# Kernel optimization log

Measured on AMD Instinct MI355X. Metric: run time of the kernel, lower is better.

## Reference

```python
import jax, jax.numpy as jnp
import numpy as np
import math

HEAD_SIZE = 64
N_EMBED = 1024
BLOCK_SIZE = 2048
BATCH = 8


def setup_inputs() -> dict:
    key = jax.random.key(0)
    k1, k2, k3, k4, k5 = jax.random.split(key, 5)
    index = jax.random.normal(k1, (BATCH, BLOCK_SIZE, N_EMBED), dtype=jnp.float32)
    memory = jax.random.normal(k2, (BATCH, BLOCK_SIZE, N_EMBED), dtype=jnp.float32)
    # torch Linear weights: [out_features, in_features], kaiming-uniform-ish init
    bound = 1.0 / math.sqrt(N_EMBED)
    Wq = jax.random.uniform(k3, (HEAD_SIZE, N_EMBED), jnp.float32, -bound, bound)
    Wk = jax.random.uniform(k4, (HEAD_SIZE, N_EMBED), jnp.float32, -bound, bound)
    Wv = jax.random.uniform(k5, (HEAD_SIZE, N_EMBED), jnp.float32, -bound, bound)
    return {"index": index, "memory": memory, "Wq": Wq, "Wk": Wk, "Wv": Wv}


def reference(index, memory, Wq, Wk, Wv):
    # q/k/v projections (Linear without bias: x @ W.T)
    q = jnp.einsum('btc,hc->bth', index, Wq)   # [B,T,H]
    k = jnp.einsum('bsc,hc->bsh', memory, Wk)  # [B,S,H]
    v = jnp.einsum('bsc,hc->bsh', memory, Wv)  # [B,S,H]
    scale = 1.0 / math.sqrt(HEAD_SIZE)
    w = jnp.einsum('bth,bsh->bts', q, k) * scale  # [B,T,S]
    # causal mask: tril==0 -> -inf
    T = index.shape[1]
    causal = jnp.tril(jnp.ones((BLOCK_SIZE, BLOCK_SIZE), dtype=bool))[:T, :T]
    w = jnp.where(causal, w, -jnp.inf)
    w = jax.nn.softmax(w, axis=-1)
    out = jnp.einsum('bts,bsh->bth', w, v)  # [B,T,H]
    return out
```

## Files before the change

kernel.cpp:

```cpp
#include <hip/hip_runtime.h>
#include <math.h>

typedef __bf16 bf16;
typedef __bf16 bf16x4 __attribute__((ext_vector_type(4)));
typedef __bf16 bf16x8 __attribute__((ext_vector_type(8)));
typedef float f32x4 __attribute__((ext_vector_type(4)));

#define MFMA16(a,b,c) __builtin_amdgcn_mfma_f32_16x16x32_bf16((a),(b),(c),0,0,0)

static constexpr int HS  = 64;
static constexpr int SEQ = 2048;
static constexpr int NE  = 1024;
static constexpr int NB  = 8;

__device__ __forceinline__ bf16x8 cvt8(float4 a, float4 b) {
  bf16x8 r;
  r[0]=(bf16)a.x; r[1]=(bf16)a.y; r[2]=(bf16)a.z; r[3]=(bf16)a.w;
  r[4]=(bf16)b.x; r[5]=(bf16)b.y; r[6]=(bf16)b.z; r[7]=(bf16)b.w;
  return r;
}

__device__ __forceinline__ void gload16(const void* g, void* l) {
  __builtin_amdgcn_global_load_lds(
      (const __attribute__((address_space(1))) void*)g,
      (__attribute__((address_space(3))) void*)l, 16, 0, 0);
}

__global__ __launch_bounds__(256) void wcvt_kernel(
    const float* __restrict__ Wq, const float* __restrict__ Wk,
    const float* __restrict__ Wv, bf16* __restrict__ wqb,
    bf16* __restrict__ wkb, bf16* __restrict__ wvb)
{
  int i = (blockIdx.x * 256 + threadIdx.x) * 4;
  float4 q = *(const float4*)(Wq + i);
  float4 k = *(const float4*)(Wk + i);
  float4 v = *(const float4*)(Wv + i);
  bf16x4 qo, ko, vo;
  qo[0]=(bf16)(q.x*0.125f); qo[1]=(bf16)(q.y*0.125f); qo[2]=(bf16)(q.z*0.125f); qo[3]=(bf16)(q.w*0.125f);
  ko[0]=(bf16)k.x; ko[1]=(bf16)k.y; ko[2]=(bf16)k.z; ko[3]=(bf16)k.w;
  vo[0]=(bf16)v.x; vo[1]=(bf16)v.y; vo[2]=(bf16)v.z; vo[3]=(bf16)v.w;
  *(bf16x4*)(wqb + i) = qo;
  *(bf16x4*)(wkb + i) = ko;
  *(bf16x4*)(wvb + i) = vo;
}

template<int KV>
__device__ __forceinline__ void proj_body(
    const float* __restrict__ X, const bf16* __restrict__ W0,
    const bf16* __restrict__ W1, bf16* __restrict__ out0,
    bf16* __restrict__ outVT, int slab,
    char* Xs0, char* Xs1, char* W0s0, char* W0s1, char* W1s0, char* W1s1)
{
  const int tid  = threadIdx.x;
  const int lane = tid & 63;
  const int w    = tid >> 6;
  const int m    = lane & 15;
  const int g    = lane >> 4;
  const int rowBase = slab * 64;

  const f32x4 vz = {0.f,0.f,0.f,0.f};
  f32x4 accA[4] = {vz, vz, vz, vz};
  f32x4 accB[4] = {vz, vz, vz, vz};

  const float* Xbase = X + (size_t)rowBase * NE;

  auto stage = [&](int kt, char* Xd, char* W0d, char* W1d) {
#pragma unroll
    for (int q = 0; q < 4; ++q) {
      int r = (q*4 + w)*4 + (lane >> 4);
      int s = lane & 15;
      const float* src = Xbase + (size_t)r * NE + kt*64 + ((s ^ (r & 15)) * 4);
      gload16(src, Xd + (q*4 + w)*1024);
    }
#pragma unroll
    for (int q = 0; q < 2; ++q) {
      int r = (q*4 + w)*8 + (lane >> 3);
      int s = lane & 7;
      size_t soff = (size_t)r * NE + kt*64 + ((s ^ (r & 7)) * 8);
      gload16(W0 + soff, W0d + (q*4 + w)*1024);
      if (KV) gload16(W1 + soff, W1d + (q*4 + w)*1024);
    }
  };

  auto compute = [&](const char* Xd, const char* W0d, const char* W1d) {
#pragma unroll
    for (int kk = 0; kk < 2; ++kk) {
      const int arow = 16*w + m;
      const int s0 = 2*(kk*4 + g);
      const char* ab = Xd + arow*256;
      float4 x0 = *(const float4*)(ab + (( s0      ^ (arow & 15)) * 16));
      float4 x1 = *(const float4*)(ab + (((s0 + 1) ^ (arow & 15)) * 16));
      bf16x8 af = cvt8(x0, x1);
#pragma unroll
      for (int n = 0; n < 4; ++n) {
        const int col = 16*n + m;
        const int ws  = kk*4 + g;
        bf16x8 b0 = *(const bf16x8*)(W0d + col*128 + ((ws ^ (col & 7)) * 16));
        accA[n] = MFMA16(af, b0, accA[n]);
        if (KV) {
          bf16x8 b1 = *(const bf16x8*)(W1d + col*128 + ((ws ^ (col & 7)) * 16));
          accB[n] = MFMA16(af, b1, accB[n]);
        }
      }
    }
  };

  stage(0, Xs0, W0s0, W1s0);
  stage(1, Xs1, W0s1, W1s1);
#pragma unroll
  for (int t = 0; t < 16; ++t) {
    if (t < 15) {
      if (KV) asm volatile("s_waitcnt vmcnt(8)" ::: "memory");
      else    asm volatile("s_waitcnt vmcnt(6)" ::: "memory");
    } else {
      asm volatile("s_waitcnt vmcnt(0)" ::: "memory");
    }
    __builtin_amdgcn_s_barrier();
    __builtin_amdgcn_sched_barrier(0);
    if ((t & 1) == 0) compute(Xs0, W0s0, W1s0);
    else              compute(Xs1, W0s1, W1s1);
    __builtin_amdgcn_sched_barrier(0);
    __builtin_amdgcn_s_barrier();
    if (t + 2 < 16) {
      if ((t & 1) == 0) stage(t + 2, Xs0, W0s0, W1s0);
      else              stage(t + 2, Xs1, W0s1, W1s1);
    }
  }

#pragma unroll
  for (int n = 0; n < 4; ++n)
#pragma unroll
    for (int i = 0; i < 4; ++i) {
      int row = rowBase + 16*w + 4*g + i;
      int h   = 16*n + m;
      out0[(size_t)row * HS + h] = (bf16)accA[n][i];
      if (KV)
        outVT[((size_t)(row >> 11) * HS + h) * SEQ + (row & 2047)] =
            (bf16)accB[n][i];
    }
}

__global__ __launch_bounds__(256, 2) void proj_kernel(
    const float* __restrict__ index, const float* __restrict__ memory,
    const bf16* __restrict__ wqb, const bf16* __restrict__ wkb,
    const bf16* __restrict__ wvb, bf16* __restrict__ qb,
    bf16* __restrict__ kb, bf16* __restrict__ vtb)
{
  __shared__ __align__(1024) char Xs0[16384], Xs1[16384];
  __shared__ __align__(1024) char W0s0[8192], W0s1[8192];
  __shared__ __align__(1024) char W1s0[8192], W1s1[8192];
  if (blockIdx.x < 256)
    proj_body<0>(index,  wqb, nullptr, qb, nullptr, blockIdx.x,
                 Xs0, Xs1, W0s0, W0s1, W1s0, W1s1);
  else
    proj_body<1>(memory, wkb, wvb,     kb, vtb, blockIdx.x - 256,
                 Xs0, Xs1, W0s0, W0s1, W1s0, W1s1);
}

__global__ __launch_bounds__(128) void attn_kernel(
    const bf16* __restrict__ qb, const bf16* __restrict__ kb,
    const bf16* __restrict__ vtb, float* __restrict__ out)
{
  __shared__ __align__(16) bf16 Ks[2][64][72];
  __shared__ __align__(16) bf16 VTs[2][64][72];
  __shared__ __align__(16) bf16 Ps[2][16][72];

  const int tid  = threadIdx.x;
  const int lane = tid & 63;
  const int w    = tid >> 6;
  const int m    = lane & 15;
  const int g    = lane >> 4;
  const int qt   = 127 - blockIdx.x;
  const int b    = blockIdx.y;
  const int nkv  = (qt >> 2) + 1;
  const int r0   = lane >> 1;
  const int hh   = (lane & 1) * 32;

  bf16x8 qf0 = *(const bf16x8*)(qb + ((size_t)b*SEQ + qt*16 + m)*HS + g*8);
  bf16x8 qf1 = *(const bf16x8*)(qb + ((size_t)b*SEQ + qt*16 + m)*HS + 32 + g*8);

  const f32x4 vz = {0.f,0.f,0.f,0.f};
  f32x4 o_acc[4] = {vz, vz, vz, vz};
  float mrun = -INFINITY, lrun = 0.f;

  bf16x8 kp[8], vp[8];
  const bf16* kbB = kb  + (size_t)b*SEQ*HS;
  const bf16* vtB = vtb + (size_t)b*HS*SEQ;

  auto loadKV = [&](int j) {
    const bf16* kt_ = kbB + (size_t)j*64*HS;
    const bf16* vt_ = vtB + j*64;
#pragma unroll
    for (int q = 0; q < 4; ++q) {
      kp[q]   = *(const bf16x8*)(kt_ + (size_t)r0*64        + hh + q*8);
      kp[4+q] = *(const bf16x8*)(kt_ + (size_t)(r0+32)*64   + hh + q*8);
      vp[q]   = *(const bf16x8*)(vt_ + (size_t)r0*SEQ       + hh + q*8);
      vp[4+q] = *(const bf16x8*)(vt_ + (size_t)(r0+32)*SEQ  + hh + q*8);
    }
  };
  auto writeKV = [&]() {
#pragma unroll
    for (int q = 0; q < 4; ++q) {
      *(bf16x8*)&Ks[w][r0][hh + q*8]      = kp[q];
      *(bf16x8*)&Ks[w][r0+32][hh + q*8]   = kp[4+q];
      *(bf16x8*)&VTs[w][r0][hh + q*8]     = vp[q];
      *(bf16x8*)&VTs[w][r0+32][hh + q*8]  = vp[4+q];
    }
  };

  int j = w;
  if (j < nkv) {
    loadKV(j);
    writeKV();
    while (true) {
      const int jn = j + 2;
      const bool more = jn < nkv;
      if (more) loadKV(jn);

      f32x4 s_acc[4];
#pragma unroll
      for (int na = 0; na < 4; ++na) {
        f32x4 z = vz;
        z = MFMA16(*(const bf16x8*)&Ks[w][16*na + m][g*8],      qf0, z);
        z = MFMA16(*(const bf16x8*)&Ks[w][16*na + m][32 + g*8], qf1, z);
        s_acc[na] = z;
      }
      if (j == nkv - 1) {
        const int q_ = qt*16 + m;
#pragma unroll
        for (int na = 0; na < 4; ++na)
#pragma unroll
          for (int i = 0; i < 4; ++i)
            if (j*64 + 16*na + 4*g + i > q_) s_acc[na][i] = -INFINITY;
      }

      float mx = fmaxf(
        fmaxf(fmaxf(fmaxf(s_acc[0][0],s_acc[0][1]),fmaxf(s_acc[0][2],s_acc[0][3])),
              fmaxf(fmaxf(s_acc[1][0],s_acc[1][1]),fmaxf(s_acc[1][2],s_acc[1][3]))),
        fmaxf(fmaxf(fmaxf(s_acc[2][0],s_acc[2][1]),fmaxf(s_acc[2][2],s_acc[2][3])),
              fmaxf(fmaxf(s_acc[3][0],s_acc[3][1]),fmaxf(s_acc[3][2],s_acc[3][3]))));
      mx = fmaxf(mx, __shfl_xor(mx, 16));
      mx = fmaxf(mx, __shfl_xor(mx, 32));
      float mnew = fmaxf(mrun, mx);
      float corr = __expf(mrun - mnew);
      mrun = mnew;
      float ts = 0.f;
#pragma unroll
      for (int na = 0; na < 4; ++na) {
        bf16x4 pk;
#pragma unroll
        for (int i = 0; i < 4; ++i) {
          float p = __expf(s_acc[na][i] - mnew);
          ts += p;
          pk[i] = (bf16)p;
        }
        *(bf16x4*)&Ps[w][m][16*na + 4*g] = pk;
      }
      ts += __shfl_xor(ts, 16);
      ts += __shfl_xor(ts, 32);
      lrun = lrun * corr + ts;
#pragma unroll
      for (int nd = 0; nd < 4; ++nd)
#pragma unroll
        for (int i = 0; i < 4; ++i) o_acc[nd][i] *= corr;

      bf16x8 pf0 = *(const bf16x8*)&Ps[w][m][g*8];
      bf16x8 pf1 = *(const bf16x8*)&Ps[w][m][32 + g*8];
#pragma unroll
      for (int nd = 0; nd < 4; ++nd) {
        o_acc[nd] = MFMA16(*(const bf16x8*)&VTs[w][16*nd + m][g*8],      pf0, o_acc[nd]);
        o_acc[nd] = MFMA16(*(const bf16x8*)&VTs[w][16*nd + m][32 + g*8], pf1, o_acc[nd]);
      }

      if (!more) break;
      writeKV();
      j = jn;
    }
  }

  float* PO = (float*)&Ks[w][0][0];
  float* PM = (float*)&VTs[w][0][0];
#pragma unroll
  for (int nd = 0; nd < 4; ++nd)
    *(f32x4*)&PO[m*68 + 16*nd + 4*g] = o_acc[nd];
  if (g == 0) { PM[m] = mrun; PM[16 + m] = lrun; }
  __syncthreads();

  {
    const int r  = tid >> 3;
    const int c0 = (tid & 7) * 8;
    const float* O0 = (const float*)&Ks[0][0][0];
    const float* O1 = (const float*)&Ks[1][0][0];
    const float* M0 = (const float*)&VTs[0][0][0];
    const float* M1 = (const float*)&VTs[1][0][0];
    float m0 = M0[r], l0 = M0[16 + r];
    float m1 = M1[r], l1 = M1[16 + r];
    float mx = fmaxf(m0, m1);
    float s0 = __expf(m0 - mx), s1 = __expf(m1 - mx);
    float inv = 1.f / (s0*l0 + s1*l1);
    float4 x0 = *(const float4*)(O0 + r*68 + c0);
    float4 x1 = *(const float4*)(O0 + r*68 + c0 + 4);
    float4 y0 = *(const float4*)(O1 + r*68 + c0);
    float4 y1 = *(const float4*)(O1 + r*68 + c0 + 4);
    float4 o0, o1;
    o0.x=(x0.x*s0+y0.x*s1)*inv; o0.y=(x0.y*s0+y0.y*s1)*inv;
    o0.z=(x0.z*s0+y0.z*s1)*inv; o0.w=(x0.w*s0+y0.w*s1)*inv;
    o1.x=(x1.x*s0+y1.x*s1)*inv; o1.y=(x1.y*s0+y1.y*s1)*inv;
    o1.z=(x1.z*s0+y1.z*s1)*inv; o1.w=(x1.w*s0+y1.w*s1)*inv;
    float* op = out + ((size_t)b*SEQ + qt*16 + r) * HS + c0;
    *(float4*)(op)     = o0;
    *(float4*)(op + 4) = o1;
  }
}

extern "C" void kernel_launch(void* const* d_in, const int* in_sizes, int n_in,
                              void* d_out, int out_size, void* d_ws, size_t ws_size,
                              hipStream_t stream) {
  (void)in_sizes; (void)n_in; (void)out_size; (void)ws_size;
  const float* index  = (const float*)d_in[0];
  const float* memory = (const float*)d_in[1];
  const float* Wq     = (const float*)d_in[2];
  const float* Wk     = (const float*)d_in[3];
  const float* Wv     = (const float*)d_in[4];
  float* out = (float*)d_out;

  bf16* qb  = (bf16*)d_ws;
  bf16* kb  = qb  + (size_t)NB * SEQ * HS;
  bf16* vtb = kb  + (size_t)NB * SEQ * HS;
  bf16* wqb = vtb + (size_t)NB * SEQ * HS;
  bf16* wkb = wqb + (size_t)HS * NE;
  bf16* wvb = wkb + (size_t)HS * NE;

  wcvt_kernel<<<dim3(64), 256, 0, stream>>>(Wq, Wk, Wv, wqb, wkb, wvb);
  proj_kernel<<<dim3(512), 256, 0, stream>>>(index, memory, wqb, wkb, wvb, qb, kb, vtb);
  attn_kernel<<<dim3(128, 8), 128, 0, stream>>>(qb, kb, vtb, out);
}
```

Before: 72.86 us.

## Stage projection tiles through registers with bf16 conversion and triple-buffered LDS

The projection kernel no longer uses direct global-to-LDS loads of fp32 X tiles. It now loads X and weights into registers, converts X to bf16 before writing it to LDS, and uses a three-stage LDS ring with register double-buffering. This halves the LDS footprint of X, removes the per-compute fp32-to-bf16 conversion, and drops one barrier per iteration. In exchange it uses more VGPRs and the stores go through registers, which may reduce overlap or occupancy.

```diff
diff --git a/kernel.cpp b/kernel.cpp
--- a/kernel.cpp
+++ b/kernel.cpp
@@ -18,12 +18,6 @@
   r[0]=(bf16)a.x; r[1]=(bf16)a.y; r[2]=(bf16)a.z; r[3]=(bf16)a.w;
   r[4]=(bf16)b.x; r[5]=(bf16)b.y; r[6]=(bf16)b.z; r[7]=(bf16)b.w;
   return r;
-}
-
-__device__ __forceinline__ void gload16(const void* g, void* l) {
-  __builtin_amdgcn_global_load_lds(
-      (const __attribute__((address_space(1))) void*)g,
-      (__attribute__((address_space(3))) void*)l, 16, 0, 0);
 }
 
 __global__ __launch_bounds__(256) void wcvt_kernel(
@@ -49,7 +43,9 @@
     const float* __restrict__ X, const bf16* __restrict__ W0,
     const bf16* __restrict__ W1, bf16* __restrict__ out0,
     bf16* __restrict__ outVT, int slab,
-    char* Xs0, char* Xs1, char* W0s0, char* W0s1, char* W1s0, char* W1s1)
+    char* Xs0, char* Xs1, char* Xs2,
+    char* W0s0, char* W0s1, char* W0s2,
+    char* W1s0, char* W1s1, char* W1s2)
 {
   const int tid  = threadIdx.x;
   const int lane = tid & 63;
@@ -57,75 +53,88 @@
   const int m    = lane & 15;
   const int g    = lane >> 4;
   const int rowBase = slab * 64;
+  const int srow = tid >> 2;
+  const int sg2  = (tid & 3) * 2;
+
+  const float* Xrow  = X  + (size_t)(rowBase + srow) * NE + (tid & 3) * 16;
+  const bf16*  W0row = W0 + (size_t)srow * NE + (tid & 3) * 16;
+  const bf16*  W1row = KV ? (W1 + (size_t)srow * NE + (tid & 3) * 16) : nullptr;
 
   const f32x4 vz = {0.f,0.f,0.f,0.f};
   f32x4 accA[4] = {vz, vz, vz, vz};
   f32x4 accB[4] = {vz, vz, vz, vz};
 
-  const float* Xbase = X + (size_t)rowBase * NE;
-
-  auto stage = [&](int kt, char* Xd, char* W0d, char* W1d) {
-#pragma unroll
-    for (int q = 0; q < 4; ++q) {
-      int r = (q*4 + w)*4 + (lane >> 4);
-      int s = lane & 15;
-      const float* src = Xbase + (size_t)r * NE + kt*64 + ((s ^ (r & 15)) * 4);
-      gload16(src, Xd + (q*4 + w)*1024);
-    }
-#pragma unroll
-    for (int q = 0; q < 2; ++q) {
-      int r = (q*4 + w)*8 + (lane >> 3);
-      int s = lane & 7;
-      size_t soff = (size_t)r * NE + kt*64 + ((s ^ (r & 7)) * 8);
-      gload16(W0 + soff, W0d + (q*4 + w)*1024);
-      if (KV) gload16(W1 + soff, W1d + (q*4 + w)*1024);
-    }
-  };
+  float4 xaA, xbA, xcA, xdA;  bf16x8 w0aA, w0bA, w1aA, w1bA;
+  float4 xaB, xbB, xcB, xdB;  bf16x8 w0aB, w0bB, w1aB, w1bB;
+
+#define LOAD_SET(S, kt) do {                                          \
+    const float* _xp = Xrow + (kt) * 64;                              \
+    xa##S = *(const float4*)(_xp);      xb##S = *(const float4*)(_xp + 4);  \
+    xc##S = *(const float4*)(_xp + 8);  xd##S = *(const float4*)(_xp + 12); \
+    const bf16* _w0 = W0row + (kt) * 64;                              \
+    w0a##S = *(const bf16x8*)(_w0);     w0b##S = *(const bf16x8*)(_w0 + 8); \
+    if (KV) { const bf16* _w1 = W1row + (kt) * 64;                    \
+      w1a##S = *(const bf16x8*)(_w1);   w1b##S = *(const bf16x8*)(_w1 + 8); } \
+  } while (0)
+
+#define WRITE_SET(S, Xd, W0d, W1d) do {                               \
+    *(bf16x8*)((Xd)  + srow*128 + 16*(( sg2   ) ^ (srow & 7))) = cvt8(xa##S, xb##S); \
+    *(bf16x8*)((Xd)  + srow*128 + 16*(( sg2+1 ) ^ (srow & 7))) = cvt8(xc##S, xd##S); \
+    *(bf16x8*)((W0d) + srow*128 + 16*(( sg2   ) ^ (srow & 7))) = w0a##S; \
+    *(bf16x8*)((W0d) + srow*128 + 16*(( sg2+1 ) ^ (srow & 7))) = w0b##S; \
+    if (KV) {                                                          \
+      *(bf16x8*)((W1d) + srow*128 + 16*(( sg2   ) ^ (srow & 7))) = w1a##S; \
+      *(bf16x8*)((W1d) + srow*128 + 16*(( sg2+1 ) ^ (srow & 7))) = w1b##S; \
+    }                                                                  \
+  } while (0)
 
   auto compute = [&](const char* Xd, const char* W0d, const char* W1d) {
 #pragma unroll
     for (int kk = 0; kk < 2; ++kk) {
       const int arow = 16*w + m;
-      const int s0 = 2*(kk*4 + g);
-      const char* ab = Xd + arow*256;
-      float4 x0 = *(const float4*)(ab + (( s0      ^ (arow & 15)) * 16));
-      float4 x1 = *(const float4*)(ab + (((s0 + 1) ^ (arow & 15)) * 16));
-      bf16x8 af = cvt8(x0, x1);
+      const int s = kk*4 + g;
+      bf16x8 af = *(const bf16x8*)(Xd + arow*128 + 16*(s ^ (arow & 7)));
 #pragma unroll
       for (int n = 0; n < 4; ++n) {
         const int col = 16*n + m;
-        const int ws  = kk*4 + g;
-        bf16x8 b0 = *(const bf16x8*)(W0d + col*128 + ((ws ^ (col & 7)) * 16));
+        bf16x8 b0 = *(const bf16x8*)(W0d + col*128 + 16*(s ^ (col & 7)));
         accA[n] = MFMA16(af, b0, accA[n]);
         if (KV) {
-          bf16x8 b1 = *(const bf16x8*)(W1d + col*128 + ((ws ^ (col & 7)) * 16));
+          bf16x8 b1 = *(const bf16x8*)(W1d + col*128 + 16*(s ^ (col & 7)));
           accB[n] = MFMA16(af, b1, accB[n]);
         }
       }
     }
   };
 
-  stage(0, Xs0, W0s0, W1s0);
-  stage(1, Xs1, W0s1, W1s1);
+  char* const XB[3]  = {Xs0,  Xs1,  Xs2};
+  char* const W0B[3] = {W0s0, W0s1, W0s2};
+  char* const W1B[3] = {W1s0, W1s1, W1s2};
+
+  LOAD_SET(A, 0);
+  LOAD_SET(B, 1);
+  WRITE_SET(A, XB[0], W0B[0], W1B[0]);
+  LOAD_SET(A, 2);
+
 #pragma unroll
   for (int t = 0; t < 16; ++t) {
+    const int wb = (t + 1) % 3;
     if (t < 15) {
-      if (KV) asm volatile("s_waitcnt vmcnt(8)" ::: "memory");
-      else    asm volatile("s_waitcnt vmcnt(6)" ::: "memory");
-    } else {
-      asm volatile("s_waitcnt vmcnt(0)" ::: "memory");
-    }
+      if (((t + 1) & 1) == 0) WRITE_SET(A, XB[wb], W0B[wb], W1B[wb]);
+      else                    WRITE_SET(B, XB[wb], W0B[wb], W1B[wb]);
+    }
+    if (t + 3 < 16) {
+      if (((t + 3) & 1) == 0) LOAD_SET(A, t + 3);
+      else                    LOAD_SET(B, t + 3);
+    }
+    __builtin_amdgcn_sched_barrier(0);
+    asm volatile("s_waitcnt lgkmcnt(0)" ::: "memory");
     __builtin_amdgcn_s_barrier();
     __builtin_amdgcn_sched_barrier(0);
-    if ((t & 1) == 0) compute(Xs0, W0s0, W1s0);
-    else              compute(Xs1, W0s1, W1s1);
-    __builtin_amdgcn_sched_barrier(0);
-    __builtin_amdgcn_s_barrier();
-    if (t + 2 < 16) {
-      if ((t & 1) == 0) stage(t + 2, Xs0, W0s0, W1s0);
-      else              stage(t + 2, Xs1, W0s1, W1s1);
-    }
+    compute(XB[t % 3], W0B[t % 3], W1B[t % 3]);
   }
+#undef LOAD_SET
+#undef WRITE_SET
 
 #pragma unroll
   for (int n = 0; n < 4; ++n)
@@ -146,15 +155,15 @@
     const bf16* __restrict__ wvb, bf16* __restrict__ qb,
     bf16* __restrict__ kb, bf16* __restrict__ vtb)
 {
-  __shared__ __align__(1024) char Xs0[16384], Xs1[16384];
-  __shared__ __align__(1024) char W0s0[8192], W0s1[8192];
-  __shared__ __align__(1024) char W1s0[8192], W1s1[8192];
+  __shared__ __align__(16) char Xs0[8192],  Xs1[8192],  Xs2[8192];
+  __shared__ __align__(16) char W0s0[8192], W0s1[8192], W0s2[8192];
+  __shared__ __align__(16) char W1s0[8192], W1s1[8192], W1s2[8192];
   if (blockIdx.x < 256)
     proj_body<0>(index,  wqb, nullptr, qb, nullptr, blockIdx.x,
-                 Xs0, Xs1, W0s0, W0s1, W1s0, W1s1);
+                 Xs0, Xs1, Xs2, W0s0, W0s1, W0s2, W1s0, W1s1, W1s2);
   else
     proj_body<1>(memory, wkb, wvb,     kb, vtb, blockIdx.x - 256,
-                 Xs0, Xs1, W0s0, W0s1, W1s0, W1s1);
+                 Xs0, Xs1, Xs2, W0s0, W0s1, W0s2, W1s0, W1s1, W1s2);
 }
 
 __global__ __launch_bounds__(128) void attn_kernel(
```

New measurement: 74.25 us. No clear change (+1.9%).

## Restructure projection kernel with register-staged bf16 LDS tiles and 128-row blocks

Applied to the files above, without the earlier changes.

The Q/K/V projection kernel drops direct global-to-LDS fp32 loads. Each thread now loads fp32 X tiles into registers, converts them to bf16, and writes them into swizzled LDS, with two register buffers and two LDS buffers double-buffered. Blocks grow to 512 threads covering 128 rows. In KV blocks, waves 0-3 compute K and waves 4-7 compute V, and Q and KV blocks are interleaved across the grid. The aim is to halve LDS footprint and traffic, move conversion out of the MFMA inner loop, and improve load balance. The cost is higher register pressure, fewer and larger blocks, and global-load latency hidden only by register prefetch.

```diff
diff --git a/kernel.cpp b/kernel.cpp
--- a/kernel.cpp
+++ b/kernel.cpp
@@ -13,17 +13,11 @@
 static constexpr int NE  = 1024;
 static constexpr int NB  = 8;
 
-__device__ __forceinline__ bf16x8 cvt8(float4 a, float4 b) {
+__device__ __forceinline__ bf16x8 cvt8v(f32x4 a, f32x4 b) {
   bf16x8 r;
-  r[0]=(bf16)a.x; r[1]=(bf16)a.y; r[2]=(bf16)a.z; r[3]=(bf16)a.w;
-  r[4]=(bf16)b.x; r[5]=(bf16)b.y; r[6]=(bf16)b.z; r[7]=(bf16)b.w;
+  r[0]=(bf16)a[0]; r[1]=(bf16)a[1]; r[2]=(bf16)a[2]; r[3]=(bf16)a[3];
+  r[4]=(bf16)b[0]; r[5]=(bf16)b[1]; r[6]=(bf16)b[2]; r[7]=(bf16)b[3];
   return r;
-}
-
-__device__ __forceinline__ void gload16(const void* g, void* l) {
-  __builtin_amdgcn_global_load_lds(
-      (const __attribute__((address_space(1))) void*)g,
-      (__attribute__((address_space(3))) void*)l, 16, 0, 0);
 }
 
 __global__ __launch_bounds__(256) void wcvt_kernel(
@@ -47,114 +41,165 @@
 template<int KV>
 __device__ __forceinline__ void proj_body(
     const float* __restrict__ X, const bf16* __restrict__ W0,
-    const bf16* __restrict__ W1, bf16* __restrict__ out0,
+    const bf16* __restrict__ W1, bf16* __restrict__ outA,
     bf16* __restrict__ outVT, int slab,
-    char* Xs0, char* Xs1, char* W0s0, char* W0s1, char* W1s0, char* W1s1)
+    bf16* __restrict__ Xs0, bf16* __restrict__ Xs1,
+    bf16* __restrict__ Ws0, bf16* __restrict__ Ws1)
 {
   const int tid  = threadIdx.x;
   const int lane = tid & 63;
   const int w    = tid >> 6;
   const int m    = lane & 15;
   const int g    = lane >> 4;
-  const int rowBase = slab * 64;
+  const int rowBase = slab * 128;
+  const int srow = tid >> 2;
+  const int sc   = tid & 3;
+  const int wrow = tid >> 3;
+  const int wseg = tid & 7;
+
+  const float* xp  = X  + (size_t)(rowBase + srow) * NE + sc * 16;
+  const bf16*  w0p = W0 + (size_t)wrow * NE + wseg * 8;
+  const bf16*  w1p = KV ? (W1 + (size_t)wrow * NE + wseg * 8) : nullptr;
 
   const f32x4 vz = {0.f,0.f,0.f,0.f};
-  f32x4 accA[4] = {vz, vz, vz, vz};
-  f32x4 accB[4] = {vz, vz, vz, vz};
-
-  const float* Xbase = X + (size_t)rowBase * NE;
-
-  auto stage = [&](int kt, char* Xd, char* W0d, char* W1d) {
-#pragma unroll
-    for (int q = 0; q < 4; ++q) {
-      int r = (q*4 + w)*4 + (lane >> 4);
-      int s = lane & 15;
-      const float* src = Xbase + (size_t)r * NE + kt*64 + ((s ^ (r & 15)) * 4);
-      gload16(src, Xd + (q*4 + w)*1024);
-    }
-#pragma unroll
-    for (int q = 0; q < 2; ++q) {
-      int r = (q*4 + w)*8 + (lane >> 3);
-      int s = lane & 7;
-      size_t soff = (size_t)r * NE + kt*64 + ((s ^ (r & 7)) * 8);
-      gload16(W0 + soff, W0d + (q*4 + w)*1024);
-      if (KV) gload16(W1 + soff, W1d + (q*4 + w)*1024);
+  f32x4 acc0[4] = {vz, vz, vz, vz};
+  f32x4 acc1[4] = {vz, vz, vz, vz};
+
+  f32x4 xaA, xbA, xcA, xdA;  bf16x8 wkA, wvA;
+  f32x4 xaB, xbB, xcB, xdB;  bf16x8 wkB, wvB;
+
+#define LOAD_T(S, kt) do {                                              \
+    const float* _p = xp + (kt) * 64;                                   \
+    xa##S = *(const f32x4*)(_p);      xb##S = *(const f32x4*)(_p + 4);  \
+    xc##S = *(const f32x4*)(_p + 8);  xd##S = *(const f32x4*)(_p + 12); \
+    wk##S = *(const bf16x8*)(w0p + (kt) * 64);                          \
+    if (KV) wv##S = *(const bf16x8*)(w1p + (kt) * 64);                  \
+    asm volatile("" : "+v"(xa##S),"+v"(xb##S),"+v"(xc##S),"+v"(xd##S)); \
+  } while (0)
+
+#define WRITE_T(S, Xd, Wk_, Wv_) do {                                     \
+    *(bf16x8*)((char*)(Xd) + srow*128 + 16*((sc*2    ) ^ (srow & 7))) =   \
+        cvt8v(xa##S, xb##S);                                              \
+    *(bf16x8*)((char*)(Xd) + srow*128 + 16*((sc*2 + 1) ^ (srow & 7))) =   \
+        cvt8v(xc##S, xd##S);                                              \
+    *(bf16x8*)((char*)(Wk_) + wrow*128 + 16*(wseg ^ (wrow & 7))) = wk##S; \
+    if (KV)                                                               \
+      *(bf16x8*)((char*)(Wv_) + wrow*128 + 16*(wseg ^ (wrow & 7))) = wv##S;\
+  } while (0)
+
+  auto compute = [&](const bf16* Xd, const bf16* Wk_, const bf16* Wv_) {
+    if (!KV) {
+      const int arow = 16*w + m;
+#pragma unroll
+      for (int kk = 0; kk < 2; ++kk) {
+        bf16x8 af = *(const bf16x8*)((const char*)Xd + arow*128 +
+                                     16*((kk*4 + g) ^ (arow & 7)));
+#pragma unroll
+        for (int n = 0; n < 4; ++n) {
+          const int col = 16*n + m;
+          bf16x8 b0 = *(const bf16x8*)((const char*)Wk_ + col*128 +
+                                       16*((kk*4 + g) ^ (col & 7)));
+          acc0[n] = MFMA16(af, b0, acc0[n]);
+        }
+      }
+    } else {
+      const int wk_ = w & 3;
+      const bf16* Wd = (w < 4) ? Wk_ : Wv_;
+#pragma unroll
+      for (int rt = 0; rt < 2; ++rt) {
+        const int arow = 32*wk_ + 16*rt + m;
+#pragma unroll
+        for (int kk = 0; kk < 2; ++kk) {
+          bf16x8 af = *(const bf16x8*)((const char*)Xd + arow*128 +
+                                       16*((kk*4 + g) ^ (arow & 7)));
+#pragma unroll
+          for (int n = 0; n < 4; ++n) {
+            const int col = 16*n + m;
+            bf16x8 b0 = *(const bf16x8*)((const char*)Wd + col*128 +
+                                         16*((kk*4 + g) ^ (col & 7)));
+            if (rt == 0) acc0[n] = MFMA16(af, b0, acc0[n]);
+            else         acc1[n] = MFMA16(af, b0, acc1[n]);
+          }
+        }
+      }
     }
   };
 
-  auto compute = [&](const char* Xd, const char* W0d, const char* W1d) {
-#pragma unroll
-    for (int kk = 0; kk < 2; ++kk) {
-      const int arow = 16*w + m;
-      const int s0 = 2*(kk*4 + g);
-      const char* ab = Xd + arow*256;
-      float4 x0 = *(const float4*)(ab + (( s0      ^ (arow & 15)) * 16));
-      float4 x1 = *(const float4*)(ab + (((s0 + 1) ^ (arow & 15)) * 16));
-      bf16x8 af = cvt8(x0, x1);
-#pragma unroll
-      for (int n = 0; n < 4; ++n) {
-        const int col = 16*n + m;
-        const int ws  = kk*4 + g;
-        bf16x8 b0 = *(const bf16x8*)(W0d + col*128 + ((ws ^ (col & 7)) * 16));
-        accA[n] = MFMA16(af, b0, accA[n]);
-        if (KV) {
-          bf16x8 b1 = *(const bf16x8*)(W1d + col*128 + ((ws ^ (col & 7)) * 16));
-          accB[n] = MFMA16(af, b1, accB[n]);
-        }
-      }
-    }
-  };
-
-  stage(0, Xs0, W0s0, W1s0);
-  stage(1, Xs1, W0s1, W1s1);
+  LOAD_T(A, 0);
+  WRITE_T(A, Xs0, Ws0, Ws0 + 64*64);
+  LOAD_T(B, 1);
+  asm volatile("s_waitcnt lgkmcnt(0)" ::: "memory");
+  __builtin_amdgcn_s_barrier();
+
 #pragma unroll
   for (int t = 0; t < 16; ++t) {
-    if (t < 15) {
-      if (KV) asm volatile("s_waitcnt vmcnt(8)" ::: "memory");
-      else    asm volatile("s_waitcnt vmcnt(6)" ::: "memory");
-    } else {
-      asm volatile("s_waitcnt vmcnt(0)" ::: "memory");
-    }
+    if ((t & 1) == 0) compute(Xs0, Ws0, Ws0 + 64*64);
+    else              compute(Xs1, Ws1, Ws1 + 64*64);
+    if (t + 2 < 16) {
+      if (((t + 2) & 1) == 0) LOAD_T(A, t + 2);
+      else                    LOAD_T(B, t + 2);
+    }
+    if (t + 1 < 16) {
+      if (((t + 1) & 1) == 0) WRITE_T(A, Xs0, Ws0, Ws0 + 64*64);
+      else                    WRITE_T(B, Xs1, Ws1, Ws1 + 64*64);
+    }
+    __builtin_amdgcn_sched_barrier(0);
+    asm volatile("s_waitcnt lgkmcnt(0)" ::: "memory");
     __builtin_amdgcn_s_barrier();
     __builtin_amdgcn_sched_barrier(0);
-    if ((t & 1) == 0) compute(Xs0, W0s0, W1s0);
-    else              compute(Xs1, W0s1, W1s1);
-    __builtin_amdgcn_sched_barrier(0);
-    __builtin_amdgcn_s_barrier();
-    if (t + 2 < 16) {
-      if ((t & 1) == 0) stage(t + 2, Xs0, W0s0, W1s0);
-      else              stage(t + 2, Xs1, W0s1, W1s1);
-    }
   }
-
-#pragma unroll
-  for (int n = 0; n < 4; ++n)
-#pragma unroll
-    for (int i = 0; i < 4; ++i) {
-      int row = rowBase + 16*w + 4*g + i;
-      int h   = 16*n + m;
-      out0[(size_t)row * HS + h] = (bf16)accA[n][i];
-      if (KV)
-        outVT[((size_t)(row >> 11) * HS + h) * SEQ + (row & 2047)] =
-            (bf16)accB[n][i];
-    }
-}
-
-__global__ __launch_bounds__(256, 2) void proj_kernel(
+#undef LOAD_T
+#undef WRITE_T
+
+  if (!KV) {
+#pragma unroll
+    for (int n = 0; n < 4; ++n)
+#pragma unroll
+      for (int i = 0; i < 4; ++i) {
+        int row = rowBase + 16*w + 4*g + i;
+        outA[(size_t)row * HS + 16*n + m] = (bf16)acc0[n][i];
+      }
+  } else if (w < 4) {
+#pragma unroll
+    for (int rt = 0; rt < 2; ++rt)
+#pragma unroll
+      for (int n = 0; n < 4; ++n)
+#pragma unroll
+        for (int i = 0; i < 4; ++i) {
+          int row = rowBase + 32*(w & 3) + 16*rt + 4*g + i;
+          f32x4& a = rt ? acc1[n] : acc0[n];
+          outA[(size_t)row * HS + 16*n + m] = (bf16)a[i];
+        }
+  } else {
+#pragma unroll
+    for (int rt = 0; rt < 2; ++rt)
+#pragma unroll
+      for (int n = 0; n < 4; ++n)
+#pragma unroll
+        for (int i = 0; i < 4; ++i) {
+          int row = rowBase + 32*(w & 3) + 16*rt + 4*g + i;
+          int h   = 16*n + m;
+          f32x4& a = rt ? acc1[n] : acc0[n];
+          outVT[((size_t)(row >> 11) * HS + h) * SEQ + (row & 2047)] =
+              (bf16)a[i];
+        }
+  }
+}
+
+__global__ __launch_bounds__(512, 4) void proj_kernel(
     const float* __restrict__ index, const float* __restrict__ memory,
     const bf16* __restrict__ wqb, const bf16* __restrict__ wkb,
     const bf16* __restrict__ wvb, bf16* __restrict__ qb,
     bf16* __restrict__ kb, bf16* __restrict__ vtb)
 {
-  __shared__ __align__(1024) char Xs0[16384], Xs1[16384];
-  __shared__ __align__(1024) char W0s0[8192], W0s1[8192];
-  __shared__ __align__(1024) char W1s0[8192], W1s1[8192];
-  if (blockIdx.x < 256)
-    proj_body<0>(index,  wqb, nullptr, qb, nullptr, blockIdx.x,
-                 Xs0, Xs1, W0s0, W0s1, W1s0, W1s1);
+  __shared__ __align__(16) bf16 Xs0[128*64], Xs1[128*64];
+  __shared__ __align__(16) bf16 Ws0[2*64*64], Ws1[2*64*64];
+  const int bid  = blockIdx.x;
+  const int slab = bid >> 1;
+  if ((bid & 1) == 0)
+    proj_body<0>(index,  wqb, nullptr, qb, nullptr, slab, Xs0, Xs1, Ws0, Ws1);
   else
-    proj_body<1>(memory, wkb, wvb,     kb, vtb, blockIdx.x - 256,
-                 Xs0, Xs1, W0s0, W0s1, W1s0, W1s1);
+    proj_body<1>(memory, wkb, wvb,     kb, vtb,     slab, Xs0, Xs1, Ws0, Ws1);
 }
 
 __global__ __launch_bounds__(128) void attn_kernel(
@@ -332,6 +377,6 @@
   bf16* wvb = wkb + (size_t)HS * NE;
 
   wcvt_kernel<<<dim3(64), 256, 0, stream>>>(Wq, Wk, Wv, wqb, wkb, wvb);
-  proj_kernel<<<dim3(512), 256, 0, stream>>>(index, memory, wqb, wkb, wvb, qb, kb, vtb);
+  proj_kernel<<<dim3(256), 512, 0, stream>>>(index, memory, wqb, wkb, wvb, qb, kb, vtb);
   attn_kernel<<<dim3(128, 8), 128, 0, stream>>>(qb, kb, vtb, out);
 }
```

Result: slower. 75.08 us (+3.1%).
